# Kernel tuning notes

Hardware: AMD Instinct MI355X
Metric: run time of the kernel (lower is better)

Reference implementation:

```python
import jax, jax.numpy as jnp
import numpy as np

H = 128   # hidden_size
B = 8
TQ = 512  # num queries
TK = 512  # num keys


def setup_inputs() -> dict:
    key = jax.random.key(0)
    ks = jax.random.split(key, 8)
    s = 1.0 / np.sqrt(H)  # torch Linear default init bound
    return {
        "queries": jax.random.normal(ks[0], (B, TQ, H), dtype=jnp.float32),
        "keys": jax.random.normal(ks[1], (B, TK, H), dtype=jnp.float32),
        "Wa_w": jax.random.uniform(ks[2], (H, H), jnp.float32, -s, s),
        "Wa_b": jax.random.uniform(ks[3], (H,), jnp.float32, -s, s),
        "Ua_w": jax.random.uniform(ks[4], (H, H), jnp.float32, -s, s),
        "Ua_b": jax.random.uniform(ks[5], (H,), jnp.float32, -s, s),
        "Va_w": jax.random.uniform(ks[6], (H,), jnp.float32, -s, s),
        "Va_b": jax.random.uniform(ks[7], (), jnp.float32, -s, s),
    }


def reference(queries, keys, Wa_w, Wa_b, Ua_w, Ua_b, Va_w, Va_b):
    # Linear projections (torch Linear: y = x @ W.T + b)
    q = queries @ Wa_w.T + Wa_b                  # (B, Tq, H)
    k = keys @ Ua_w.T + Ua_b                     # (B, Tk, H)
    # Additive (Bahdanau) scores with broadcast intermediate (B, Tq, Tk, H)
    e = jnp.tanh(q[:, :, None, :] + k[:, None, :, :])
    scores = jnp.einsum('bqkh,h->bqk', e, Va_w) + Va_b  # (B, Tq, Tk)
    weights = jax.nn.softmax(scores, axis=-1)            # softmax over keys
    contexts = jnp.einsum('bqk,bkh->bqh', weights, keys) # (B, Tq, H)
    return contexts, weights
```

## Files before the change

### kernel.cpp

```cpp
#include <hip/hip_runtime.h>
#include <hip/hip_bf16.h>
#include <stdint.h>

#define HD 128
#define NB 8
#define TQN 512
#define TKN 512
#define QT 8
#define KTILE 64
#define KSTR 132
#define QSTR 132
#define KBSTR 136

typedef __attribute__((ext_vector_type(8))) short short8;
typedef __attribute__((ext_vector_type(4))) float f32x4;
typedef __attribute__((ext_vector_type(2))) float f32x2;

#if __has_builtin(__builtin_elementwise_fma)
#define FMA2(a,b,c) __builtin_elementwise_fma((a),(b),(c))
#else
#define FMA2(a,b,c) ((a)*(b)+(c))
#endif

static __device__ __forceinline__ float lo16(uint32_t w){
  union { uint32_t i; float f; } v; v.i = w << 16; return v.f;
}
static __device__ __forceinline__ float hi16(uint32_t w){
  union { uint32_t i; float f; } v; v.i = w & 0xffff0000u; return v.f;
}
static __device__ __forceinline__ float bf2f(unsigned short u){
  union { uint32_t i; float f; } v; v.i = ((uint32_t)u) << 16; return v.f;
}
static __device__ __forceinline__ uint32_t f2bf(float f){
  union { float f; uint32_t i; } v; v.f = f;
  uint32_t u = v.i;
  u += 0x7fffu + ((u >> 16) & 1u);
  return u >> 16;
}
static __device__ __forceinline__ float tanh_acc(float x){
  float e = __builtin_amdgcn_exp2f(x * 2.8853900817779268f);
  return fmaf(-2.0f, __builtin_amdgcn_rcpf(e + 1.0f), 1.0f);
}
template<int CTRL>
static __device__ __forceinline__ float dpp_add(float x){
  union { float f; int i; } u; u.f = x;
  int y = __builtin_amdgcn_update_dpp(0, u.i, CTRL, 0xf, 0xf, true);
  union { int i; float f; } w; w.i = y;
  return x + w.f;
}
static __device__ __forceinline__ float ld1(const void* p, size_t idx, bool f32){
  return f32 ? ((const float*)p)[idx] : bf2f(((const unsigned short*)p)[idx]);
}
static __device__ __forceinline__ short8 ld8bf(const void* p, size_t idx, bool f32){
  short8 r;
  if (f32){
    const float* s = (const float*)p + idx;
    #pragma unroll
    for (int i = 0; i < 8; i++) r[i] = (short)f2bf(s[i]);
  } else {
    r = *(const short8*)((const unsigned short*)p + idx);
  }
  return r;
}

__global__ __launch_bounds__(256) void proj_kernel(
    const void* __restrict__ queries, const void* __restrict__ keys,
    const void* __restrict__ Wa_w,   const void* __restrict__ Wa_b,
    const void* __restrict__ Ua_w,   const void* __restrict__ Ua_b,
    float* __restrict__ tq_g, float* __restrict__ tk_g)
{
  __shared__ unsigned int flg_s[8];
  const int tid = threadIdx.x;
  if (tid < 8) flg_s[tid] = 0;
  __syncthreads();
  {
    const void* ptrs[6] = {queries, keys, Wa_w, Wa_b, Ua_w, Ua_b};
    const int grp = tid >> 5;
    const int l   = tid & 31;
    if (grp < 6){
      const unsigned short* p = (const unsigned short*)ptrs[grp];
      unsigned short a = p[2*l], c = p[64 + 2*l];
      if (((a >> 7) & 0xFF) > 0x90 || ((c >> 7) & 0xFF) > 0x90)
        atomicOr(&flg_s[grp], 1u);
    }
  }
  __syncthreads();
  const int lane = tid & 63, wv = tid >> 6, ln = lane & 15, quad = lane >> 4;
  const int b7  = blockIdx.x & 7;
  const int idx = blockIdx.x >> 3;
  const int row0 = (idx < 32) ? (b7*TQN + idx*16)
                              : (NB*TQN + b7*TKN + (idx-32)*16);

  const void* x; const void* W; const void* bias; float* dst; int r;
  bool fx, fw, fb;
  if (row0 < NB*TQN){
    x = queries; W = Wa_w; bias = Wa_b; dst = tq_g; r = row0;
    fx = flg_s[0] != 0; fw = flg_s[2] != 0; fb = flg_s[3] != 0;
  } else {
    x = keys; W = Ua_w; bias = Ua_b; dst = tk_g; r = row0 - NB*TQN;
    fx = flg_s[1] != 0; fw = flg_s[4] != 0; fb = flg_s[5] != 0;
  }

  short8 a[4];
  #pragma unroll
  for (int ks = 0; ks < 4; ks++)
    a[ks] = ld8bf(x, (size_t)(r + ln)*HD + ks*32 + quad*8, fx);

  #pragma unroll
  for (int nt = 0; nt < 2; nt++){
    const int h0 = (2*wv + nt)*16;
    f32x4 c = {0.f,0.f,0.f,0.f};
    #pragma unroll
    for (int ks = 0; ks < 4; ks++)
      c = __builtin_amdgcn_mfma_f32_16x16x32_bf16(
            a[ks], ld8bf(W, (size_t)(h0 + ln)*HD + ks*32 + quad*8, fw), c, 0,0,0);
    const float wb = ld1(bias, h0 + ln, fb);
    #pragma unroll
    for (int r4 = 0; r4 < 4; r4++)
      dst[(size_t)(r + quad*4 + r4)*HD + h0 + ln] = tanh_acc(c[r4] + wb);
  }
}

__global__ __launch_bounds__(512, 4) void attn_kernel(
    const void* __restrict__ queries, const void* __restrict__ keys,
    const void* __restrict__ Va_w,
    const float* __restrict__ tq_g, const float* __restrict__ tk_g,
    void* __restrict__ out)
{
  __shared__ __align__(16) float tk_s[KTILE*KSTR];
  __shared__ float sc_s[QT*TKN];
  __shared__ unsigned int flg_s[4];

  const int tid = threadIdx.x;
  const int b     = blockIdx.x & 7;
  const int qbase = (blockIdx.x >> 3) * QT;

  float4 st[4];
  {
    const float4* src = (const float4*)(tk_g + (size_t)(b*TKN)*HD);
    #pragma unroll
    for (int j = 0; j < 4; j++) st[j] = src[tid + 512*j];
  }

  if (tid < 4) flg_s[tid] = 0;
  __syncthreads();
  {
    const void* ptrs[3] = {queries, keys, Va_w};
    const int grp = tid >> 5;
    const int l   = tid & 31;
    if (grp < 3){
      const unsigned short* p = (const unsigned short*)ptrs[grp];
      unsigned short a = p[2*l], c = p[64 + 2*l];
      if (((a >> 7) & 0xFF) > 0x90 || ((c >> 7) & 0xFF) > 0x90)
        atomicOr(&flg_s[grp], 1u);
    }
  }
  __syncthreads();
  const bool fQ  = flg_s[0] != 0;
  const bool fK  = flg_s[1] != 0;
  const bool fVw = flg_s[2] != 0;

  const int lane = tid & 63;
  const int wv   = tid >> 6;
  const int ln   = lane & 15;
  const int quad = lane >> 4;
  const int s8   = lane >> 3;
  const int o8   = lane & 7;

  f32x2 var2[8], tq2[8], vat2[8];
  {
    float vtmp[16];
    #pragma unroll
    for (int j = 0; j < 16; j++) vtmp[j] = ld1(Va_w, o8*16 + j, fVw);
    const float4* qsrc = (const float4*)(tq_g + (size_t)(b*TQN + qbase + wv)*HD + o8*16);
    #pragma unroll
    for (int c = 0; c < 4; c++){
      float4 t = qsrc[c];
      f32x2 t0; t0.x = t.x; t0.y = t.y;
      f32x2 t1; t1.x = t.z; t1.y = t.w;
      f32x2 v0; v0.x = vtmp[4*c+0]; v0.y = vtmp[4*c+1];
      f32x2 v1; v1.x = vtmp[4*c+2]; v1.y = vtmp[4*c+3];
      tq2[2*c] = t0;  tq2[2*c+1] = t1;
      var2[2*c] = v0; var2[2*c+1] = v1;
      vat2[2*c] = v0 * t0; vat2[2*c+1] = v1 * t1;
    }
  }
  f32x2 one2; one2.x = 1.f; one2.y = 1.f;

  float sc8[8];
  for (int kt = 0; kt < 8; kt++){
    #pragma unroll
    for (int j = 0; j < 4; j++){
      const int f = tid + 512*j;
      *(float4*)(tk_s + (f >> 5)*KSTR + (f & 31)*4) = st[j];
    }
    __syncthreads();
    if (kt < 7){
      const float4* src = (const float4*)(tk_g + (size_t)(b*TKN + (kt+1)*KTILE)*HD);
      #pragma unroll
      for (int j = 0; j < 4; j++) st[j] = src[tid + 512*j];
    }

    f32x2 acc2[8];
    #pragma unroll
    for (int i = 0; i < 8; i++){ acc2[i].x = 0.f; acc2[i].y = 0.f; }
    #pragma unroll
    for (int i = 0; i < 8; i++){
      const float* tk = tk_s + (i*8 + s8)*KSTR + o8*16;
      #pragma unroll
      for (int c = 0; c < 4; c++){
        const float4 kv = *(const float4*)(tk + c*4);
        f32x2 kv0; kv0.x = kv.x; kv0.y = kv.y;
        f32x2 kv1; kv1.x = kv.z; kv1.y = kv.w;
        f32x2 n0 = FMA2(var2[2*c],   kv0, vat2[2*c]);
        f32x2 d0 = FMA2(tq2[2*c],    kv0, one2);
        f32x2 n1 = FMA2(var2[2*c+1], kv1, vat2[2*c+1]);
        f32x2 d1 = FMA2(tq2[2*c+1],  kv1, one2);
        f32x2 r0; r0.x = __builtin_amdgcn_rcpf(d0.x); r0.y = __builtin_amdgcn_rcpf(d0.y);
        f32x2 r1; r1.x = __builtin_amdgcn_rcpf(d1.x); r1.y = __builtin_amdgcn_rcpf(d1.y);
        acc2[i] = FMA2(n0, r0, acc2[i]);
        acc2[i] = FMA2(n1, r1, acc2[i]);
      }
    }
    float ar[8];
    #pragma unroll
    for (int i = 0; i < 8; i++){
      float a = acc2[i].x + acc2[i].y;
      a = dpp_add<0xB1>(a);
      a = dpp_add<0x4E>(a);
      a = dpp_add<0x141>(a);
      ar[i] = a;
    }
    float sc = ar[0];
    #pragma unroll
    for (int i = 1; i < 8; i++) sc = (o8 == i) ? ar[i] : sc;
    sc8[kt] = sc;
    __syncthreads();
  }

  uint4 kf[4];
  if (fK){
    const uint4* src = (const uint4*)((const float*)keys + (size_t)(b*TKN)*HD);
    #pragma unroll
    for (int j = 0; j < 4; j++) kf[j] = src[tid + 512*j];
  } else {
    const uint4* src = (const uint4*)((const unsigned short*)keys + (size_t)(b*TKN)*HD);
    #pragma unroll
    for (int j = 0; j < 2; j++) kf[j] = src[tid + 512*j];
  }

  {
    float m = sc8[0];
    #pragma unroll
    for (int j = 1; j < 8; j++) m = fmaxf(m, sc8[j]);
    #pragma unroll
    for (int o = 32; o > 0; o >>= 1) m = fmaxf(m, __shfl_xor(m, o));
    float sum = 0.f;
    #pragma unroll
    for (int j = 0; j < 8; j++){
      sc8[j] = __builtin_amdgcn_exp2f((sc8[j]-m)*1.4426950408889634f);
      sum += sc8[j];
    }
    #pragma unroll
    for (int o = 32; o > 0; o >>= 1) sum += __shfl_xor(sum, o);
    const float inv = __builtin_amdgcn_rcpf(sum);
    const int psrc = ((((lane & 7) << 3) | (lane >> 3)) << 2);
    const size_t wbase = (size_t)NB*TQN*HD + (size_t)(b*TQN + qbase + wv)*TKN;
    #pragma unroll
    for (int j = 0; j < 8; j++){
      union { float f; int i; } u; u.f = sc8[j]*inv;
      union { int i; float f; } t; t.i = __builtin_amdgcn_ds_bpermute(psrc, u.i);
      sc_s[wv*TKN + j*64 + lane] = t.f;
      if (fQ) ((float*)out)[wbase + j*64 + lane] = t.f;
      else    ((unsigned short*)out)[wbase + j*64 + lane] = (unsigned short)f2bf(t.f);
    }
  }
  __syncthreads();

  {
    const int p2 = wv & 3;
    const int g2 = wv >> 2;
    const int h0 = ln * 8;
    f32x2 a0v[4], a1v[4];
    #pragma unroll
    for (int t = 0; t < 4; t++){
      a0v[t].x = 0.f; a0v[t].y = 0.f;
      a1v[t].x = 0.f; a1v[t].y = 0.f;
    }
    for (int kt = 0; kt < 8; kt++){
      if (fK){
        #pragma unroll
        for (int j = 0; j < 4; j++){
          const int f = tid + 512*j;
          float4 v;
          v.x = __uint_as_float(kf[j].x); v.y = __uint_as_float(kf[j].y);
          v.z = __uint_as_float(kf[j].z); v.w = __uint_as_float(kf[j].w);
          *(float4*)(tk_s + (f >> 5)*KSTR + (f & 31)*4) = v;
        }
      } else {
        #pragma unroll
        for (int j = 0; j < 2; j++){
          const int f = tid + 512*j;
          const int k = f >> 4;
          const int h = (f & 15) * 8;
          uint4 v = kf[j];
          float4 d0, d1;
          d0.x = lo16(v.x); d0.y = hi16(v.x); d0.z = lo16(v.y); d0.w = hi16(v.y);
          d1.x = lo16(v.z); d1.y = hi16(v.z); d1.z = lo16(v.w); d1.w = hi16(v.w);
          *(float4*)(tk_s + k*KSTR + h)     = d0;
          *(float4*)(tk_s + k*KSTR + h + 4) = d1;
        }
      }
      __syncthreads();
      if (kt < 7){
        if (fK){
          const uint4* src = (const uint4*)((const float*)keys + (size_t)(b*TKN + (kt+1)*KTILE)*HD);
          #pragma unroll
          for (int j = 0; j < 4; j++) kf[j] = src[tid + 512*j];
        } else {
          const uint4* src = (const uint4*)((const unsigned short*)keys + (size_t)(b*TKN + (kt+1)*KTILE)*HD);
          #pragma unroll
          for (int j = 0; j < 2; j++) kf[j] = src[tid + 512*j];
        }
      }
      const float* w0r = sc_s + (2*p2)*TKN + kt*KTILE + g2*32;
      const float* w1r = w0r + TKN;
      #pragma unroll
      for (int i = 0; i < 8; i++){
        const int k = i*4 + quad;
        const float w0 = w0r[k];
        const float w1 = w1r[k];
        const float* kr = tk_s + (g2*32 + k)*KSTR + h0;
        const float4 k0 = *(const float4*)(kr);
        const float4 k1 = *(const float4*)(kr + 4);
        f32x2 c0; c0.x = k0.x; c0.y = k0.y;
        f32x2 c1; c1.x = k0.z; c1.y = k0.w;
        f32x2 c2; c2.x = k1.x; c2.y = k1.y;
        f32x2 c3; c3.x = k1.z; c3.y = k1.w;
        f32x2 w0v; w0v.x = w0; w0v.y = w0;
        f32x2 w1v; w1v.x = w1; w1v.y = w1;
        a0v[0] = FMA2(w0v, c0, a0v[0]); a0v[1] = FMA2(w0v, c1, a0v[1]);
        a0v[2] = FMA2(w0v, c2, a0v[2]); a0v[3] = FMA2(w0v, c3, a0v[3]);
        a1v[0] = FMA2(w1v, c0, a1v[0]); a1v[1] = FMA2(w1v, c1, a1v[1]);
        a1v[2] = FMA2(w1v, c2, a1v[2]); a1v[3] = FMA2(w1v, c3, a1v[3]);
      }
      __syncthreads();
    }
    float a0[8], a1[8];
    #pragma unroll
    for (int t = 0; t < 4; t++){
      a0[2*t] = a0v[t].x; a0[2*t+1] = a0v[t].y;
      a1[2*t] = a1v[t].x; a1[2*t+1] = a1v[t].y;
    }
    #pragma unroll
    for (int t = 0; t < 8; t++){
      a0[t] += __shfl_xor(a0[t], 16); a0[t] += __shfl_xor(a0[t], 32);
      a1[t] += __shfl_xor(a1[t], 16); a1[t] += __shfl_xor(a1[t], 32);
    }
    float* part = sc_s;
    if (g2 == 1 && quad == 0){
      *(float4*)(part + (2*p2  )*HD + h0    ) = (float4){a0[0],a0[1],a0[2],a0[3]};
      *(float4*)(part + (2*p2  )*HD + h0 + 4) = (float4){a0[4],a0[5],a0[6],a0[7]};
      *(float4*)(part + (2*p2+1)*HD + h0    ) = (float4){a1[0],a1[1],a1[2],a1[3]};
      *(float4*)(part + (2*p2+1)*HD + h0 + 4) = (float4){a1[4],a1[5],a1[6],a1[7]};
    }
    __syncthreads();
    if (g2 == 0 && quad == 0){
      const float4 p00 = *(const float4*)(part + (2*p2  )*HD + h0    );
      const float4 p01 = *(const float4*)(part + (2*p2  )*HD + h0 + 4);
      const float4 p10 = *(const float4*)(part + (2*p2+1)*HD + h0    );
      const float4 p11 = *(const float4*)(part + (2*p2+1)*HD + h0 + 4);
      const size_t crow0 = (size_t)(b*TQN + qbase + 2*p2    )*HD + h0;
      const size_t crow1 = (size_t)(b*TQN + qbase + 2*p2 + 1)*HD + h0;
      if (fQ){
        float* oc = (float*)out;
        *(float4*)(oc + crow0)     = (float4){a0[0]+p00.x, a0[1]+p00.y, a0[2]+p00.z, a0[3]+p00.w};
        *(float4*)(oc + crow0 + 4) = (float4){a0[4]+p01.x, a0[5]+p01.y, a0[6]+p01.z, a0[7]+p01.w};
        *(float4*)(oc + crow1)     = (float4){a1[0]+p10.x, a1[1]+p10.y, a1[2]+p10.z, a1[3]+p10.w};
        *(float4*)(oc + crow1 + 4) = (float4){a1[4]+p11.x, a1[5]+p11.y, a1[6]+p11.z, a1[7]+p11.w};
      } else {
        uint4 o0, o1;
        o0.x = f2bf(a0[0]+p00.x) | (f2bf(a0[1]+p00.y) << 16);
        o0.y = f2bf(a0[2]+p00.z) | (f2bf(a0[3]+p00.w) << 16);
        o0.z = f2bf(a0[4]+p01.x) | (f2bf(a0[5]+p01.y) << 16);
        o0.w = f2bf(a0[6]+p01.z) | (f2bf(a0[7]+p01.w) << 16);
        o1.x = f2bf(a1[0]+p10.x) | (f2bf(a1[1]+p10.y) << 16);
        o1.y = f2bf(a1[2]+p10.z) | (f2bf(a1[3]+p10.w) << 16);
        o1.z = f2bf(a1[4]+p11.x) | (f2bf(a1[5]+p11.y) << 16);
        o1.w = f2bf(a1[6]+p11.z) | (f2bf(a1[7]+p11.w) << 16);
        *(uint4*)((unsigned short*)out + crow0) = o0;
        *(uint4*)((unsigned short*)out + crow1) = o1;
      }
    }
  }
}

__global__ __launch_bounds__(512, 4) void fused_kernel(
    const void* __restrict__ queries, const void* __restrict__ keys,
    const void* __restrict__ Wa_w,   const void* __restrict__ Wa_b,
    const void* __restrict__ Ua_w,   const void* __restrict__ Ua_b,
    const void* __restrict__ Va_w,
    void* __restrict__ out)
{
  __shared__ float qp_s[QT*QSTR];
  __shared__ float va_s[HD];
  __shared__ __align__(16) unsigned short keys_s[KTILE*KBSTR];
  __shared__ __align__(16) float kp_s[KTILE*KSTR];
  __shared__ float sc_s[QT*TKN];
  __shared__ unsigned int flg_s[8];

  const int tid = threadIdx.x;
  if (tid < 8) flg_s[tid] = 0;
  __syncthreads();
  {
    const void* ptrs[7] = {queries, keys, Wa_w, Wa_b, Ua_w, Ua_b, Va_w};
    const int grp = tid >> 5;
    const int l   = tid & 31;
    if (grp < 7){
      const unsigned short* p = (const unsigned short*)ptrs[grp];
      unsigned short a = p[2*l], c = p[64 + 2*l];
      if (((a >> 7) & 0xFF) > 0x90 || ((c >> 7) & 0xFF) > 0x90)
        atomicOr(&flg_s[grp], 1u);
    }
  }
  __syncthreads();
  const bool fQ  = flg_s[0] != 0;
  const bool fK  = flg_s[1] != 0;
  const bool fWw = flg_s[2] != 0;
  const bool fWb = flg_s[3] != 0;
  const bool fUw = flg_s[4] != 0;
  const bool fUb = flg_s[5] != 0;
  const bool fVw = flg_s[6] != 0;

  const int lane = tid & 63;
  const int wv   = tid >> 6;
  const int ln   = lane & 15;
  const int quad = lane >> 4;
  const int b     = blockIdx.x >> 6;
  const int qbase = (blockIdx.x & 63) * QT;

  if (tid < HD) va_s[tid] = ld1(Va_w, tid, fVw);
  {
    const int h0 = wv * 16;
    const size_t qrow = (size_t)(b*TQN + qbase + (ln & 7))*HD;
    f32x4 c = {0.f,0.f,0.f,0.f};
    #pragma unroll
    for (int ks = 0; ks < 4; ks++){
      short8 a = ld8bf(queries, qrow + ks*32 + quad*8, fQ);
      short8 w = ld8bf(Wa_w, (size_t)(h0 + ln)*HD + ks*32 + quad*8, fWw);
      c = __builtin_amdgcn_mfma_f32_16x16x32_bf16(a, w, c, 0,0,0);
    }
    const float wb = ld1(Wa_b, h0 + ln, fWb);
    #pragma unroll
    for (int r = 0; r < 4; r++){
      const int row = quad*4 + r;
      if (row < QT) qp_s[row*QSTR + h0 + ln] = tanh_acc(c[r] + wb);
    }
  }
  short8 ub[4];
  float ubias;
  {
    const int h0 = wv * 16;
    #pragma unroll
    for (int ks = 0; ks < 4; ks++)
      ub[ks] = ld8bf(Ua_w, (size_t)(h0 + ln)*HD + ks*32 + quad*8, fUw);
    ubias = ld1(Ua_b, h0 + ln, fUb);
  }
  {
    if (fK){
      const float4* src = (const float4*)((const float*)keys + (size_t)(b*TKN)*HD);
      #pragma unroll
      for (int j = 0; j < 4; j++){
        const int f = tid + 512*j;
        float4 v = src[f];
        const int k = f >> 5, h = (f & 31)*4;
        uint2 p;
        p.x = f2bf(v.x) | (f2bf(v.y) << 16);
        p.y = f2bf(v.z) | (f2bf(v.w) << 16);
        *(uint2*)(keys_s + k*KBSTR + h) = p;
      }
    } else {
      const uint4* src = (const uint4*)((const unsigned short*)keys + (size_t)(b*TKN)*HD);
      #pragma unroll
      for (int j = 0; j < 2; j++){
        const int f = tid + 512*j;
        uint4 v = src[f];
        const int k = f >> 4, h = (f & 15)*8;
        *(uint4*)(keys_s + k*KBSTR + h) = v;
      }
    }
  }
  __syncthreads();

  const int s8 = lane >> 3;
  const int o8 = lane & 7;
  float tqr[16], var[16], vat[16];
  {
    const float* qsrc = qp_s + wv*QSTR + o8*16;
    const float* vsrc = va_s + o8*16;
    #pragma unroll
    for (int c = 0; c < 4; c++){
      float4 t = *(const float4*)(qsrc + c*4);
      float4 v = *(const float4*)(vsrc + c*4);
      tqr[c*4+0]=t.x; tqr[c*4+1]=t.y; tqr[c*4+2]=t.z; tqr[c*4+3]=t.w;
      var[c*4+0]=v.x; var[c*4+1]=v.y; var[c*4+2]=v.z; var[c*4+3]=v.w;
      vat[c*4+0]=v.x*t.x; vat[c*4+1]=v.y*t.y; vat[c*4+2]=v.z*t.z; vat[c*4+3]=v.w*t.w;
    }
  }
  for (int kt = 0; kt < 8; kt++){
    f32x4 kc[4];
    #pragma unroll
    for (int mt = 0; mt < 4; mt++) kc[mt] = (f32x4){0.f,0.f,0.f,0.f};
    #pragma unroll
    for (int ks = 0; ks < 4; ks++){
      short8 af[4];
      #pragma unroll
      for (int mt = 0; mt < 4; mt++)
        af[mt] = *(const short8*)(keys_s + (mt*16 + ln)*KBSTR + ks*32 + quad*8);
      #pragma unroll
      for (int mt = 0; mt < 4; mt++)
        kc[mt] = __builtin_amdgcn_mfma_f32_16x16x32_bf16(af[mt], ub[ks], kc[mt], 0,0,0);
    }
    __syncthreads();
    #pragma unroll
    for (int mt = 0; mt < 4; mt++)
      #pragma unroll
      for (int r = 0; r < 4; r++)
        kp_s[(mt*16 + quad*4 + r)*KSTR + wv*16 + ln] = tanh_acc(kc[mt][r] + ubias);
    if (kt < 7){
      if (fK){
        const float4* src = (const float4*)((const float*)keys + (size_t)(b*TKN + (kt+1)*KTILE)*HD);
        #pragma unroll
        for (int j = 0; j < 4; j++){
          const int f = tid + 512*j;
          float4 v = src[f];
          const int k = f >> 5, h = (f & 31)*4;
          uint2 p;
          p.x = f2bf(v.x) | (f2bf(v.y) << 16);
          p.y = f2bf(v.z) | (f2bf(v.w) << 16);
          *(uint2*)(keys_s + k*KBSTR + h) = p;
        }
      } else {
        const uint4* src = (const uint4*)((const unsigned short*)keys + (size_t)(b*TKN + (kt+1)*KTILE)*HD);
        #pragma unroll
        for (int j = 0; j < 2; j++){
          const int f = tid + 512*j;
          uint4 v = src[f];
          const int k = f >> 4, h = (f & 15)*8;
          *(uint4*)(keys_s + k*KBSTR + h) = v;
        }
      }
    }
    __syncthreads();
    float acc[8];
    #pragma unroll
    for (int i = 0; i < 8; i++) acc[i] = 0.f;
    #pragma unroll
    for (int i = 0; i < 8; i++){
      const float* tk = kp_s + (i*8 + s8)*KSTR + o8*16;
      #pragma unroll
      for (int c = 0; c < 4; c++){
        const float4 kv = *(const float4*)(tk + c*4);
        acc[i] = fmaf(fmaf(var[c*4+0], kv.x, vat[c*4+0]),
                      __builtin_amdgcn_rcpf(fmaf(tqr[c*4+0], kv.x, 1.f)), acc[i]);
        acc[i] = fmaf(fmaf(var[c*4+1], kv.y, vat[c*4+1]),
                      __builtin_amdgcn_rcpf(fmaf(tqr[c*4+1], kv.y, 1.f)), acc[i]);
        acc[i] = fmaf(fmaf(var[c*4+2], kv.z, vat[c*4+2]),
                      __builtin_amdgcn_rcpf(fmaf(tqr[c*4+2], kv.z, 1.f)), acc[i]);
        acc[i] = fmaf(fmaf(var[c*4+3], kv.w, vat[c*4+3]),
                      __builtin_amdgcn_rcpf(fmaf(tqr[c*4+3], kv.w, 1.f)), acc[i]);
      }
    }
    #pragma unroll
    for (int i = 0; i < 8; i++){
      float a = acc[i];
      a = dpp_add<0xB1>(a);
      a = dpp_add<0x4E>(a);
      a = dpp_add<0x141>(a);
      acc[i] = a;
    }
    float sc = acc[0];
    #pragma unroll
    for (int i = 1; i < 8; i++) sc = (o8 == i) ? acc[i] : sc;
    sc_s[wv*TKN + kt*KTILE + o8*8 + s8] = sc;
  }
  __syncthreads();
  {
    float vals[8];
    float m = -1e30f;
    #pragma unroll
    for (int j = 0; j < 8; j++){
      vals[j] = sc_s[wv*TKN + lane + 64*j];
      m = fmaxf(m, vals[j]);
    }
    #pragma unroll
    for (int o = 32; o > 0; o >>= 1) m = fmaxf(m, __shfl_xor(m, o));
    float sum = 0.f;
    #pragma unroll
    for (int j = 0; j < 8; j++){
      vals[j] = __builtin_amdgcn_exp2f((vals[j]-m)*1.4426950408889634f);
      sum += vals[j];
    }
    #pragma unroll
    for (int o = 32; o > 0; o >>= 1) sum += __shfl_xor(sum, o);
    const float inv = __builtin_amdgcn_rcpf(sum);
    const size_t wbase = (size_t)NB*TQN*HD + (size_t)(b*TQN + qbase + wv)*TKN;
    #pragma unroll
    for (int j = 0; j < 8; j++){
      const float w = vals[j]*inv;
      sc_s[wv*TKN + lane + 64*j] = w;
      if (fQ) ((float*)out)[wbase + lane + 64*j] = w;
      else    ((unsigned short*)out)[wbase + lane + 64*j] = (unsigned short)f2bf(w);
    }
  }
  __syncthreads();
  {
    const int p2 = wv & 3;
    const int g2 = wv >> 2;
    const int h0 = ln * 8;
    float a0[8], a1[8];
    #pragma unroll
    for (int t = 0; t < 8; t++){ a0[t] = 0.f; a1[t] = 0.f; }
    for (int kt = 0; kt < 8; kt++){
      if (fK){
        const float4* src = (const float4*)((const float*)keys + (size_t)(b*TKN + kt*KTILE)*HD);
        #pragma unroll
        for (int j = 0; j < 4; j++){
          const int f = tid + 512*j;
          const int k = f >> 5, h = (f & 31)*4;
          *(float4*)(kp_s + k*KSTR + h) = src[f];
        }
      } else {
        const uint4* src = (const uint4*)((const unsigned short*)keys + (size_t)(b*TKN + kt*KTILE)*HD);
        #pragma unroll
        for (int j = 0; j < 2; j++){
          const int f = tid + 512*j;
          const int k = f >> 4, h = (f & 15)*8;
          uint4 v = src[f];
          float4 d0, d1;
          d0.x = lo16(v.x); d0.y = hi16(v.x); d0.z = lo16(v.y); d0.w = hi16(v.y);
          d1.x = lo16(v.z); d1.y = hi16(v.z); d1.z = lo16(v.w); d1.w = hi16(v.w);
          *(float4*)(kp_s + k*KSTR + h)     = d0;
          *(float4*)(kp_s + k*KSTR + h + 4) = d1;
        }
      }
      __syncthreads();
      const float* w0r = sc_s + (2*p2)*TKN + kt*KTILE + g2*32;
      const float* w1r = w0r + TKN;
      #pragma unroll
      for (int i = 0; i < 8; i++){
        const int k = i*4 + quad;
        const float w0 = w0r[k];
        const float w1 = w1r[k];
        const float* kr = kp_s + (g2*32 + k)*KSTR + h0;
        const float4 k0 = *(const float4*)(kr);
        const float4 k1 = *(const float4*)(kr + 4);
        a0[0]=fmaf(w0,k0.x,a0[0]); a0[1]=fmaf(w0,k0.y,a0[1]);
        a0[2]=fmaf(w0,k0.z,a0[2]); a0[3]=fmaf(w0,k0.w,a0[3]);
        a0[4]=fmaf(w0,k1.x,a0[4]); a0[5]=fmaf(w0,k1.y,a0[5]);
        a0[6]=fmaf(w0,k1.z,a0[6]); a0[7]=fmaf(w0,k1.w,a0[7]);
        a1[0]=fmaf(w1,k0.x,a1[0]); a1[1]=fmaf(w1,k0.y,a1[1]);
        a1[2]=fmaf(w1,k0.z,a1[2]); a1[3]=fmaf(w1,k0.w,a1[3]);
        a1[4]=fmaf(w1,k1.x,a1[4]); a1[5]=fmaf(w1,k1.y,a1[5]);
        a1[6]=fmaf(w1,k1.z,a1[6]); a1[7]=fmaf(w1,k1.w,a1[7]);
      }
      __syncthreads();
    }
    #pragma unroll
    for (int t = 0; t < 8; t++){
      a0[t] += __shfl_xor(a0[t], 16); a0[t] += __shfl_xor(a0[t], 32);
      a1[t] += __shfl_xor(a1[t], 16); a1[t] += __shfl_xor(a1[t], 32);
    }
    float* part = qp_s;
    if (g2 == 1 && quad == 0){
      *(float4*)(part + (2*p2  )*HD + h0    ) = (float4){a0[0],a0[1],a0[2],a0[3]};
      *(float4*)(part + (2*p2  )*HD + h0 + 4) = (float4){a0[4],a0[5],a0[6],a0[7]};
      *(float4*)(part + (2*p2+1)*HD + h0    ) = (float4){a1[0],a1[1],a1[2],a1[3]};
      *(float4*)(part + (2*p2+1)*HD + h0 + 4) = (float4){a1[4],a1[5],a1[6],a1[7]};
    }
    __syncthreads();
    if (g2 == 0 && quad == 0){
      const float4 p00 = *(const float4*)(part + (2*p2  )*HD + h0    );
      const float4 p01 = *(const float4*)(part + (2*p2  )*HD + h0 + 4);
      const float4 p10 = *(const float4*)(part + (2*p2+1)*HD + h0    );
      const float4 p11 = *(const float4*)(part + (2*p2+1)*HD + h0 + 4);
      const size_t crow0 = (size_t)(b*TQN + qbase + 2*p2    )*HD + h0;
      const size_t crow1 = (size_t)(b*TQN + qbase + 2*p2 + 1)*HD + h0;
      if (fQ){
        float* oc = (float*)out;
        *(float4*)(oc + crow0)     = (float4){a0[0]+p00.x, a0[1]+p00.y, a0[2]+p00.z, a0[3]+p00.w};
        *(float4*)(oc + crow0 + 4) = (float4){a0[4]+p01.x, a0[5]+p01.y, a0[6]+p01.z, a0[7]+p01.w};
        *(float4*)(oc + crow1)     = (float4){a1[0]+p10.x, a1[1]+p10.y, a1[2]+p10.z, a1[3]+p10.w};
        *(float4*)(oc + crow1 + 4) = (float4){a1[4]+p11.x, a1[5]+p11.y, a1[6]+p11.z, a1[7]+p11.w};
      } else {
        uint4 o0, o1;
        o0.x = f2bf(a0[0]+p00.x) | (f2bf(a0[1]+p00.y) << 16);
        o0.y = f2bf(a0[2]+p00.z) | (f2bf(a0[3]+p00.w) << 16);
        o0.z = f2bf(a0[4]+p01.x) | (f2bf(a0[5]+p01.y) << 16);
        o0.w = f2bf(a0[6]+p01.z) | (f2bf(a0[7]+p01.w) << 16);
        o1.x = f2bf(a1[0]+p10.x) | (f2bf(a1[1]+p10.y) << 16);
        o1.y = f2bf(a1[2]+p10.z) | (f2bf(a1[3]+p10.w) << 16);
        o1.z = f2bf(a1[4]+p11.x) | (f2bf(a1[5]+p11.y) << 16);
        o1.w = f2bf(a1[6]+p11.z) | (f2bf(a1[7]+p11.w) << 16);
        *(uint4*)((unsigned short*)out + crow0) = o0;
        *(uint4*)((unsigned short*)out + crow1) = o1;
      }
    }
  }
}

extern "C" void kernel_launch(void* const* d_in, const int* in_sizes, int n_in,
                              void* d_out, int out_size, void* d_ws, size_t ws_size,
                              hipStream_t stream) {
  (void)in_sizes; (void)n_in; (void)out_size;
  const size_t need = (size_t)2 * NB * TQN * HD * sizeof(float);
  if (ws_size >= need){
    float* tq_g = (float*)d_ws;
    float* tk_g = tq_g + (size_t)NB*TQN*HD;
    proj_kernel<<<512, 256, 0, stream>>>(d_in[0], d_in[1], d_in[2], d_in[3],
                                         d_in[4], d_in[5], tq_g, tk_g);
    attn_kernel<<<512, 512, 0, stream>>>(d_in[0], d_in[1], d_in[6],
                                         tq_g, tk_g, d_out);
  } else {
    fused_kernel<<<512, 512, 0, stream>>>(d_in[0], d_in[1], d_in[2], d_in[3],
                                          d_in[4], d_in[5], d_in[6], d_out);
  }
}
```

Measured before the change: 149.2 us.

## Share reciprocals across four hidden dims and read keys directly from global

The projection kernel now stores exp(2x) clamped to a bounded range instead of tanh. The score loop rewrites tanh(q+k) as 1 - 2/(1+e^{2q}e^{2k}) and merges four such fractions into a single numerator/denominator, so it needs one rcp per four hidden elements rather than one per element. The lane-to-hidden mapping also changes to strided float4 reads. The context accumulation drops the LDS staging of key tiles and their barriers and loads keys straight from global/L2 per thread. The risks are overflow or precision loss in the product of four denominators, which the clamp is meant to bound, and more uncoalesced global traffic in the second phase.

```diff
diff --git a/kernel.cpp b/kernel.cpp
--- a/kernel.cpp
+++ b/kernel.cpp
@@ -116,8 +116,11 @@
             a[ks], ld8bf(W, (size_t)(h0 + ln)*HD + ks*32 + quad*8, fw), c, 0,0,0);
     const float wb = ld1(bias, h0 + ln, fb);
     #pragma unroll
-    for (int r4 = 0; r4 < 4; r4++)
-      dst[(size_t)(r + quad*4 + r4)*HD + h0 + ln] = tanh_acc(c[r4] + wb);
+    for (int r4 = 0; r4 < 4; r4++){
+      const float e = __builtin_amdgcn_exp2f((c[r4] + wb) * 2.8853900817779268f);
+      dst[(size_t)(r + quad*4 + r4)*HD + h0 + ln] =
+          fminf(fmaxf(e, 0x1p-13f), 0x1p13f);
+    }
   }
 }
 
@@ -167,22 +170,18 @@
   const int s8   = lane >> 3;
   const int o8   = lane & 7;
 
-  f32x2 var2[8], tq2[8], vat2[8];
-  {
-    float vtmp[16];
-    #pragma unroll
-    for (int j = 0; j < 16; j++) vtmp[j] = ld1(Va_w, o8*16 + j, fVw);
-    const float4* qsrc = (const float4*)(tq_g + (size_t)(b*TQN + qbase + wv)*HD + o8*16);
+  f32x2 eq2[8], a2[8];
+  {
+    const float* qsrc = tq_g + (size_t)(b*TQN + qbase + wv)*HD;
     #pragma unroll
     for (int c = 0; c < 4; c++){
-      float4 t = qsrc[c];
-      f32x2 t0; t0.x = t.x; t0.y = t.y;
-      f32x2 t1; t1.x = t.z; t1.y = t.w;
-      f32x2 v0; v0.x = vtmp[4*c+0]; v0.y = vtmp[4*c+1];
-      f32x2 v1; v1.x = vtmp[4*c+2]; v1.y = vtmp[4*c+3];
-      tq2[2*c] = t0;  tq2[2*c+1] = t1;
-      var2[2*c] = v0; var2[2*c+1] = v1;
-      vat2[2*c] = v0 * t0; vat2[2*c+1] = v1 * t1;
+      const float4 t = *(const float4*)(qsrc + c*32 + o8*4);
+      eq2[2*c].x = t.x; eq2[2*c].y = t.y;
+      eq2[2*c+1].x = t.z; eq2[2*c+1].y = t.w;
+      a2[2*c].x   = -2.0f * ld1(Va_w, c*32 + o8*4 + 0, fVw);
+      a2[2*c].y   = -2.0f * ld1(Va_w, c*32 + o8*4 + 1, fVw);
+      a2[2*c+1].x = -2.0f * ld1(Va_w, c*32 + o8*4 + 2, fVw);
+      a2[2*c+1].y = -2.0f * ld1(Va_w, c*32 + o8*4 + 3, fVw);
     }
   }
   f32x2 one2; one2.x = 1.f; one2.y = 1.f;
@@ -201,52 +200,45 @@
       for (int j = 0; j < 4; j++) st[j] = src[tid + 512*j];
     }
 
-    f32x2 acc2[8];
-    #pragma unroll
-    for (int i = 0; i < 8; i++){ acc2[i].x = 0.f; acc2[i].y = 0.f; }
+    float acc[8];
     #pragma unroll
     for (int i = 0; i < 8; i++){
-      const float* tk = tk_s + (i*8 + s8)*KSTR + o8*16;
+      const float* tk = tk_s + (i*8 + s8)*KSTR + o8*4;
+      float acci = 0.f;
       #pragma unroll
       for (int c = 0; c < 4; c++){
-        const float4 kv = *(const float4*)(tk + c*4);
+        const float4 kv = *(const float4*)(tk + c*32);
         f32x2 kv0; kv0.x = kv.x; kv0.y = kv.y;
         f32x2 kv1; kv1.x = kv.z; kv1.y = kv.w;
-        f32x2 n0 = FMA2(var2[2*c],   kv0, vat2[2*c]);
-        f32x2 d0 = FMA2(tq2[2*c],    kv0, one2);
-        f32x2 n1 = FMA2(var2[2*c+1], kv1, vat2[2*c+1]);
-        f32x2 d1 = FMA2(tq2[2*c+1],  kv1, one2);
-        f32x2 r0; r0.x = __builtin_amdgcn_rcpf(d0.x); r0.y = __builtin_amdgcn_rcpf(d0.y);
-        f32x2 r1; r1.x = __builtin_amdgcn_rcpf(d1.x); r1.y = __builtin_amdgcn_rcpf(d1.y);
-        acc2[i] = FMA2(n0, r0, acc2[i]);
-        acc2[i] = FMA2(n1, r1, acc2[i]);
-      }
-    }
-    float ar[8];
+        f32x2 x01 = FMA2(eq2[2*c],   kv0, one2);
+        f32x2 x23 = FMA2(eq2[2*c+1], kv1, one2);
+        f32x2 xs01; xs01.x = x01.y; xs01.y = x01.x;
+        f32x2 xs23; xs23.x = x23.y; xs23.y = x23.x;
+        f32x2 s01 = a2[2*c]   * xs01;
+        f32x2 s23 = a2[2*c+1] * xs23;
+        const float p01 = x01.x * x01.y;
+        const float p23 = x23.x * x23.y;
+        const float n01 = s01.x + s01.y;
+        const float n23 = s23.x + s23.y;
+        const float P   = p01 * p23;
+        const float N   = fmaf(n01, p23, n23 * p01);
+        acci = fmaf(N, __builtin_amdgcn_rcpf(P), acci);
+      }
+      acc[i] = acci;
+    }
     #pragma unroll
     for (int i = 0; i < 8; i++){
-      float a = acc2[i].x + acc2[i].y;
+      float a = acc[i];
       a = dpp_add<0xB1>(a);
       a = dpp_add<0x4E>(a);
       a = dpp_add<0x141>(a);
-      ar[i] = a;
-    }
-    float sc = ar[0];
-    #pragma unroll
-    for (int i = 1; i < 8; i++) sc = (o8 == i) ? ar[i] : sc;
+      acc[i] = a;
+    }
+    float sc = acc[0];
+    #pragma unroll
+    for (int i = 1; i < 8; i++) sc = (o8 == i) ? acc[i] : sc;
     sc8[kt] = sc;
     __syncthreads();
-  }
-
-  uint4 kf[4];
-  if (fK){
-    const uint4* src = (const uint4*)((const float*)keys + (size_t)(b*TKN)*HD);
-    #pragma unroll
-    for (int j = 0; j < 4; j++) kf[j] = src[tid + 512*j];
-  } else {
-    const uint4* src = (const uint4*)((const unsigned short*)keys + (size_t)(b*TKN)*HD);
-    #pragma unroll
-    for (int j = 0; j < 2; j++) kf[j] = src[tid + 512*j];
   }
 
   {
@@ -287,64 +279,56 @@
       a0v[t].x = 0.f; a0v[t].y = 0.f;
       a1v[t].x = 0.f; a1v[t].y = 0.f;
     }
-    for (int kt = 0; kt < 8; kt++){
-      if (fK){
+    const float* w0rb = sc_s + (2*p2)*TKN + g2*32;
+    if (!fK){
+      const unsigned short* kb = (const unsigned short*)keys
+          + (size_t)(b*TKN + g2*32)*HD + h0;
+      for (int kt = 0; kt < 8; kt++){
+        const float* w0r = w0rb + kt*KTILE;
+        const float* w1r = w0r + TKN;
         #pragma unroll
-        for (int j = 0; j < 4; j++){
-          const int f = tid + 512*j;
-          float4 v;
-          v.x = __uint_as_float(kf[j].x); v.y = __uint_as_float(kf[j].y);
-          v.z = __uint_as_float(kf[j].z); v.w = __uint_as_float(kf[j].w);
-          *(float4*)(tk_s + (f >> 5)*KSTR + (f & 31)*4) = v;
+        for (int i = 0; i < 8; i++){
+          const int k = i*4 + quad;
+          const uint4 v = *(const uint4*)(kb + (size_t)(kt*KTILE + k)*HD);
+          const float w0 = w0r[k];
+          const float w1 = w1r[k];
+          f32x2 c0; c0.x = lo16(v.x); c0.y = hi16(v.x);
+          f32x2 c1; c1.x = lo16(v.y); c1.y = hi16(v.y);
+          f32x2 c2; c2.x = lo16(v.z); c2.y = hi16(v.z);
+          f32x2 c3; c3.x = lo16(v.w); c3.y = hi16(v.w);
+          f32x2 w0v; w0v.x = w0; w0v.y = w0;
+          f32x2 w1v; w1v.x = w1; w1v.y = w1;
+          a0v[0] = FMA2(w0v, c0, a0v[0]); a0v[1] = FMA2(w0v, c1, a0v[1]);
+          a0v[2] = FMA2(w0v, c2, a0v[2]); a0v[3] = FMA2(w0v, c3, a0v[3]);
+          a1v[0] = FMA2(w1v, c0, a1v[0]); a1v[1] = FMA2(w1v, c1, a1v[1]);
+          a1v[2] = FMA2(w1v, c2, a1v[2]); a1v[3] = FMA2(w1v, c3, a1v[3]);
         }
-      } else {
+      }
+    } else {
+      const float* kb = (const float*)keys + (size_t)(b*TKN + g2*32)*HD + h0;
+      for (int kt = 0; kt < 8; kt++){
+        const float* w0r = w0rb + kt*KTILE;
+        const float* w1r = w0r + TKN;
         #pragma unroll
-        for (int j = 0; j < 2; j++){
-          const int f = tid + 512*j;
-          const int k = f >> 4;
-          const int h = (f & 15) * 8;
-          uint4 v = kf[j];
-          float4 d0, d1;
-          d0.x = lo16(v.x); d0.y = hi16(v.x); d0.z = lo16(v.y); d0.w = hi16(v.y);
-          d1.x = lo16(v.z); d1.y = hi16(v.z); d1.z = lo16(v.w); d1.w = hi16(v.w);
-          *(float4*)(tk_s + k*KSTR + h)     = d0;
-          *(float4*)(tk_s + k*KSTR + h + 4) = d1;
+        for (int i = 0; i < 8; i++){
+          const int k = i*4 + quad;
+          const float* kr = kb + (size_t)(kt*KTILE + k)*HD;
+          const float4 k0 = *(const float4*)(kr);
+          const float4 k1 = *(const float4*)(kr + 4);
+          const float w0 = w0r[k];
+          const float w1 = w1r[k];
+          f32x2 c0; c0.x = k0.x; c0.y = k0.y;
+          f32x2 c1; c1.x = k0.z; c1.y = k0.w;
+          f32x2 c2; c2.x = k1.x; c2.y = k1.y;
+          f32x2 c3; c3.x = k1.z; c3.y = k1.w;
+          f32x2 w0v; w0v.x = w0; w0v.y = w0;
+          f32x2 w1v; w1v.x = w1; w1v.y = w1;
+          a0v[0] = FMA2(w0v, c0, a0v[0]); a0v[1] = FMA2(w0v, c1, a0v[1]);
+          a0v[2] = FMA2(w0v, c2, a0v[2]); a0v[3] = FMA2(w0v, c3, a0v[3]);
+          a1v[0] = FMA2(w1v, c0, a1v[0]); a1v[1] = FMA2(w1v, c1, a1v[1]);
+          a1v[2] = FMA2(w1v, c2, a1v[2]); a1v[3] = FMA2(w1v, c3, a1v[3]);
         }
       }
-      __syncthreads();
-      if (kt < 7){
-        if (fK){
-          const uint4* src = (const uint4*)((const float*)keys + (size_t)(b*TKN + (kt+1)*KTILE)*HD);
-          #pragma unroll
-          for (int j = 0; j < 4; j++) kf[j] = src[tid + 512*j];
-        } else {
-          const uint4* src = (const uint4*)((const unsigned short*)keys + (size_t)(b*TKN + (kt+1)*KTILE)*HD);
-          #pragma unroll
-          for (int j = 0; j < 2; j++) kf[j] = src[tid + 512*j];
-        }
-      }
-      const float* w0r = sc_s + (2*p2)*TKN + kt*KTILE + g2*32;
-      const float* w1r = w0r + TKN;
-      #pragma unroll
-      for (int i = 0; i < 8; i++){
-        const int k = i*4 + quad;
-        const float w0 = w0r[k];
-        const float w1 = w1r[k];
-        const float* kr = tk_s + (g2*32 + k)*KSTR + h0;
-        const float4 k0 = *(const float4*)(kr);
-        const float4 k1 = *(const float4*)(kr + 4);
-        f32x2 c0; c0.x = k0.x; c0.y = k0.y;
-        f32x2 c1; c1.x = k0.z; c1.y = k0.w;
-        f32x2 c2; c2.x = k1.x; c2.y = k1.y;
-        f32x2 c3; c3.x = k1.z; c3.y = k1.w;
-        f32x2 w0v; w0v.x = w0; w0v.y = w0;
-        f32x2 w1v; w1v.x = w1; w1v.y = w1;
-        a0v[0] = FMA2(w0v, c0, a0v[0]); a0v[1] = FMA2(w0v, c1, a0v[1]);
-        a0v[2] = FMA2(w0v, c2, a0v[2]); a0v[3] = FMA2(w0v, c3, a0v[3]);
-        a1v[0] = FMA2(w1v, c0, a1v[0]); a1v[1] = FMA2(w1v, c1, a1v[1]);
-        a1v[2] = FMA2(w1v, c2, a1v[2]); a1v[3] = FMA2(w1v, c3, a1v[3]);
-      }
-      __syncthreads();
     }
     float a0[8], a1[8];
     #pragma unroll
@@ -357,6 +341,7 @@
       a0[t] += __shfl_xor(a0[t], 16); a0[t] += __shfl_xor(a0[t], 32);
       a1[t] += __shfl_xor(a1[t], 16); a1[t] += __shfl_xor(a1[t], 32);
     }
+    __syncthreads();
     float* part = sc_s;
     if (g2 == 1 && quad == 0){
       *(float4*)(part + (2*p2  )*HD + h0    ) = (float4){a0[0],a0[1],a0[2],a0[3]};
```

After: 149.1 us. Within noise of the previous version (-0.1%).
